# Kernel optimization log

Hardware: AMD Instinct MI355X
Metric: run time of the kernel (lower is better)

The kernel has to match this reference:

```python
import jax, jax.numpy as jnp
import numpy as np

B, S_CTX, S_Q, D_CTX, D_Q = 16, 2048, 2048, 1024, 1024
MASK_P = 0.1  # fraction of masked context positions


def setup_inputs() -> dict:
    key = jax.random.key(0)
    k1, k2, k3, k4 = jax.random.split(key, 4)
    context = jax.random.normal(k1, (B, S_CTX, D_CTX), dtype=jnp.float32)
    query = jax.random.normal(k2, (S_Q, B, D_Q), dtype=jnp.float32)  # [q_steps, batch, query_size]
    W = jax.random.normal(k3, (D_CTX, D_Q), dtype=jnp.float32)       # learned bilinear weights
    context_mask = jax.random.uniform(k4, (B, S_CTX)) < MASK_P       # True = masked position
    return {"context": context, "query": query, "W": W, "context_mask": context_mask}


def reference(context, query, W, context_mask):
    # scores[b, q, s] = context[b, s, :] @ W @ query[q, b, :]   (temp = 1.0, so no scaling)
    cw = jnp.einsum('bsd,de->bse', context, W)            # [B, S_ctx, D_q]
    scores = jnp.einsum('bse,qbe->bqs', cw, query)        # [B, S_q, S_ctx]
    neg = jnp.asarray(-1e30, scores.dtype)                # finite stand-in for -inf (NaN-safe)
    scores = jnp.where(context_mask[:, None, :], neg, scores)
    attn = jax.nn.softmax(scores, axis=2)                 # [B, S_q, S_ctx]
    # rows where the whole context is masked get attention zeroed out
    all_masked = jnp.all(context_mask, axis=1)[:, None, None]
    attn = jnp.where(all_masked, jnp.asarray(0.0, attn.dtype), attn)
    composition = jnp.einsum('bqs,bsd->qbd', attn, context)  # [S_q, B, D_ctx]
    attn_out = attn.transpose(1, 0, 2)                       # [S_q, B, S_ctx]
    return attn_out, composition
```

## Files before the change

kernel.cpp:

```cpp
#include <hip/hip_runtime.h>
#include <cmath>

#define B_  16
#define SEQ 2048
#define DIM 1024
#define LDST 40

typedef short  short8 __attribute__((ext_vector_type(8)));
typedef float  f32x4  __attribute__((ext_vector_type(4)));

__device__ __forceinline__ unsigned short f2bf(float x) {
  unsigned u = __builtin_bit_cast(unsigned, x);
  return (unsigned short)((u + 0x7fffu + ((u >> 16) & 1u)) >> 16);
}
__device__ __forceinline__ float bf2f(unsigned short h) {
  unsigned u = ((unsigned)h) << 16;
  return __builtin_bit_cast(float, u);
}

__device__ __forceinline__ void gl16(const void* g, void* l) {
  __builtin_amdgcn_global_load_lds(
      (const __attribute__((address_space(1))) void*)g,
      (__attribute__((address_space(3))) void*)l, 16, 0, 0);
}

__global__ __launch_bounds__(256) void cvt_ctx(const float* __restrict__ X,
                                               unsigned short* __restrict__ hi,
                                               unsigned short* __restrict__ lo) {
  const size_t N8 = (size_t)B_ * SEQ * DIM / 8;
  for (size_t i = (size_t)blockIdx.x * 256 + threadIdx.x; i < N8;
       i += (size_t)gridDim.x * 256) {
    const size_t base = i * 8;
    float4 a = *(const float4*)&X[base];
    float4 c = *(const float4*)&X[base + 4];
    const float xs[8] = {a.x, a.y, a.z, a.w, c.x, c.y, c.z, c.w};
    short8 h, l;
#pragma unroll
    for (int j = 0; j < 8; ++j) {
      unsigned short hh = f2bf(xs[j]);
      h[j] = (short)hh;
      l[j] = (short)f2bf(xs[j] - bf2f(hh));
    }
    *(short8*)&hi[base] = h;
    *(short8*)&lo[base] = l;
  }
}

__global__ __launch_bounds__(256) void g1_z(const float* __restrict__ Q,
                                            const float* __restrict__ W,
                                            unsigned short* __restrict__ zhi,
                                            unsigned short* __restrict__ zlo) {
  __shared__ unsigned short Ah[128 * LDST], Al[128 * LDST];
  __shared__ unsigned short Bh[128 * LDST], Bl[128 * LDST];
  const int tid = threadIdx.x;
  const int m0 = blockIdx.y * 128, n0 = blockIdx.x * 128;
  const int wave = tid >> 6, lane = tid & 63;
  const int wm = (wave >> 1) * 64, wn = (wave & 1) * 64;
  const int rl = tid & 127;

  const float* srow = (tid < 128) ? Q + (size_t)(m0 + rl) * DIM
                                  : W + (size_t)(n0 + rl) * DIM;
  unsigned short* th = (tid < 128) ? Ah : Bh;
  unsigned short* tl = (tid < 128) ? Al : Bl;

  f32x4 acc[4][4];
#pragma unroll
  for (int i = 0; i < 4; ++i)
#pragma unroll
    for (int j = 0; j < 4; ++j) acc[i][j] = (f32x4){0.f, 0.f, 0.f, 0.f};

  for (int kc = 0; kc < DIM; kc += 32) {
    float4 fv[8];
#pragma unroll
    for (int j = 0; j < 8; ++j) fv[j] = *(const float4*)&srow[kc + j * 4];
    __syncthreads();
    short8 hv[4], lv[4];
#pragma unroll
    for (int j = 0; j < 8; ++j) {
      const float x[4] = {fv[j].x, fv[j].y, fv[j].z, fv[j].w};
#pragma unroll
      for (int c = 0; c < 4; ++c) {
        unsigned short h = f2bf(x[c]);
        unsigned short l = f2bf(x[c] - bf2f(h));
        hv[j >> 1][(j & 1) * 4 + c] = (short)h;
        lv[j >> 1][(j & 1) * 4 + c] = (short)l;
      }
    }
#pragma unroll
    for (int j = 0; j < 4; ++j) {
      *(short8*)&th[rl * LDST + j * 8] = hv[j];
      *(short8*)&tl[rl * LDST + j * 8] = lv[j];
    }
    __syncthreads();

    short8 ah[4], al[4], bh[4], bl[4];
#pragma unroll
    for (int f = 0; f < 4; ++f) {
      const int ao = (wm + f * 16 + (lane & 15)) * LDST + (lane >> 4) * 8;
      const int bo = (wn + f * 16 + (lane & 15)) * LDST + (lane >> 4) * 8;
      ah[f] = *(const short8*)&Ah[ao];  al[f] = *(const short8*)&Al[ao];
      bh[f] = *(const short8*)&Bh[bo];  bl[f] = *(const short8*)&Bl[bo];
    }
#pragma unroll
    for (int i = 0; i < 4; ++i)
#pragma unroll
      for (int j = 0; j < 4; ++j) {
        acc[i][j] = __builtin_amdgcn_mfma_f32_16x16x32_bf16(ah[i], bh[j], acc[i][j], 0, 0, 0);
        acc[i][j] = __builtin_amdgcn_mfma_f32_16x16x32_bf16(al[i], bh[j], acc[i][j], 0, 0, 0);
        acc[i][j] = __builtin_amdgcn_mfma_f32_16x16x32_bf16(ah[i], bl[j], acc[i][j], 0, 0, 0);
      }
  }
#pragma unroll
  for (int i = 0; i < 4; ++i)
#pragma unroll
    for (int j = 0; j < 4; ++j)
#pragma unroll
      for (int r = 0; r < 4; ++r) {
        const int row = m0 + wm + i * 16 + (lane >> 4) * 4 + r;
        const int col = n0 + wn + j * 16 + (lane & 15);
        const float v = acc[i][j][r];
        const unsigned short h = f2bf(v);
        zhi[(size_t)row * DIM + col] = h;
        zlo[(size_t)row * DIM + col] = f2bf(v - bf2f(h));
      }
}

#define G2GRID (16 * 16 * B_)
__global__ __launch_bounds__(256) void g2_scores(const unsigned short* __restrict__ zhi,
                                                 const unsigned short* __restrict__ zlo,
                                                 const unsigned short* __restrict__ chi,
                                                 const unsigned short* __restrict__ clo,
                                                 float* __restrict__ Sc) {
  __shared__ unsigned short Sh[128 * 32], Sl[128 * 32];
  __shared__ unsigned short Qh[128 * 32], Ql[128 * 32];
  const int tid = threadIdx.x, lane = tid & 63, wave = tid >> 6;

  const int lin = blockIdx.x;
  const int swz = (lin & 7) * (G2GRID / 8) + (lin >> 3);
  const int s0 = (swz & 15) * 128;
  const int q0 = ((swz >> 4) & 15) * 128;
  const int b  = swz >> 8;

  const int wm = (wave >> 1) * 64;
  const int wn = (wave & 1) * 64;

  const int r_sub = lane >> 2;
  const int c_sub = (lane & 3) * 8;

  f32x4 acc[4][4];
#pragma unroll
  for (int i = 0; i < 4; ++i)
#pragma unroll
    for (int j = 0; j < 4; ++j) acc[i][j] = (f32x4){0.f, 0.f, 0.f, 0.f};

  for (int kc = 0; kc < DIM; kc += 32) {
    if (wave == 0) {
#pragma unroll
      for (int it = 0; it < 8; ++it)
        gl16(&chi[((size_t)b * SEQ + s0 + it * 16 + r_sub) * DIM + kc + c_sub], &Sh[it * 512]);
    } else if (wave == 1) {
#pragma unroll
      for (int it = 0; it < 8; ++it)
        gl16(&clo[((size_t)b * SEQ + s0 + it * 16 + r_sub) * DIM + kc + c_sub], &Sl[it * 512]);
    } else if (wave == 2) {
#pragma unroll
      for (int it = 0; it < 8; ++it)
        gl16(&zhi[((size_t)(q0 + it * 16 + r_sub) * B_ + b) * DIM + kc + c_sub], &Qh[it * 512]);
    } else {
#pragma unroll
      for (int it = 0; it < 8; ++it)
        gl16(&zlo[((size_t)(q0 + it * 16 + r_sub) * B_ + b) * DIM + kc + c_sub], &Ql[it * 512]);
    }
    __syncthreads();

    const int fo = lane & 15, fk = (lane >> 4) * 8;
    short8 sh_[4], sl_[4], qh_[4], ql_[4];
#pragma unroll
    for (int f = 0; f < 4; ++f) {
      const int so = (wm + f * 16 + fo) * 32 + fk;
      const int qo = (wn + f * 16 + fo) * 32 + fk;
      sh_[f] = *(const short8*)&Sh[so];  sl_[f] = *(const short8*)&Sl[so];
      qh_[f] = *(const short8*)&Qh[qo];  ql_[f] = *(const short8*)&Ql[qo];
    }
#pragma unroll
    for (int i = 0; i < 4; ++i)
#pragma unroll
      for (int j = 0; j < 4; ++j) {
        acc[i][j] = __builtin_amdgcn_mfma_f32_16x16x32_bf16(sh_[i], qh_[j], acc[i][j], 0, 0, 0);
        acc[i][j] = __builtin_amdgcn_mfma_f32_16x16x32_bf16(sl_[i], qh_[j], acc[i][j], 0, 0, 0);
        acc[i][j] = __builtin_amdgcn_mfma_f32_16x16x32_bf16(sh_[i], ql_[j], acc[i][j], 0, 0, 0);
      }
    __syncthreads();
  }

#pragma unroll
  for (int i = 0; i < 4; ++i)
#pragma unroll
    for (int j = 0; j < 4; ++j) {
      const int s = s0 + wm + i * 16 + (lane >> 4) * 4;
      const int q = q0 + wn + j * 16 + (lane & 15);
      f32x4 v = {acc[i][j][0], acc[i][j][1], acc[i][j][2], acc[i][j][3]};
      __builtin_nontemporal_store(v, (f32x4*)&Sc[((size_t)q * B_ + b) * SEQ + s]);
    }
}

__global__ __launch_bounds__(256) void kernel_softmax(float* __restrict__ attn,
                                                      const int* __restrict__ mask,
                                                      unsigned short* __restrict__ attnb) {
  const int row = blockIdx.x;
  const int b = row & (B_ - 1);
  const int q = row >> 4;
  float* p = attn + (size_t)row * SEQ;
  const int* m = mask + (size_t)b * SEQ;
  unsigned short* pb = attnb + ((size_t)b * SEQ + q) * SEQ;
  const int t = threadIdx.x;

  float v[8];
  float mx = -INFINITY;
#pragma unroll
  for (int i = 0; i < 8; ++i) {
    const int s = t + i * 256;
    float x = p[s];
    x = m[s] ? -1e30f : x;
    v[i] = x;
    mx = fmaxf(mx, x);
  }
#pragma unroll
  for (int off = 32; off > 0; off >>= 1) mx = fmaxf(mx, __shfl_xor(mx, off));
  __shared__ float redmax[4];
  __shared__ float redsum[4];
  if ((t & 63) == 0) redmax[t >> 6] = mx;
  __syncthreads();
  mx = fmaxf(fmaxf(redmax[0], redmax[1]), fmaxf(redmax[2], redmax[3]));

  float sum = 0.f;
#pragma unroll
  for (int i = 0; i < 8; ++i) {
    v[i] = __expf(v[i] - mx);
    sum += v[i];
  }
#pragma unroll
  for (int off = 32; off > 0; off >>= 1) sum += __shfl_xor(sum, off);
  if ((t & 63) == 0) redsum[t >> 6] = sum;
  __syncthreads();
  sum = (redsum[0] + redsum[1]) + (redsum[2] + redsum[3]);

  const bool allmasked = (mx < -1e29f);
  const float inv = allmasked ? 0.f : 1.f / sum;
#pragma unroll
  for (int i = 0; i < 8; ++i) {
    const float a = v[i] * inv;
    p[t + i * 256] = a;
    pb[t + i * 256] = f2bf(a);
  }
}

__global__ __launch_bounds__(256) void g3_comp(const unsigned short* __restrict__ attnb,
                                               const float* __restrict__ Ctx,
                                               float* __restrict__ Out) {
  __shared__ unsigned short As[128 * LDST], Bs[128 * LDST];
  const int b = blockIdx.z;
  const int tid = threadIdx.x;
  const int q0 = blockIdx.y * 128, d0 = blockIdx.x * 128;
  const int wave = tid >> 6, lane = tid & 63;
  const int wm = (wave >> 1) * 64, wn = (wave & 1) * 64;

  const int arow = tid >> 1, ak = (tid & 1) * 16;
  const int dl = tid & 127, sh = tid >> 7;

  const unsigned short* asrc = attnb + ((size_t)b * SEQ + (q0 + arow)) * SEQ + ak;
  const float* bsrc = Ctx + (size_t)b * SEQ * DIM + d0 + dl;

  f32x4 acc[4][4];
#pragma unroll
  for (int i = 0; i < 4; ++i)
#pragma unroll
    for (int j = 0; j < 4; ++j) acc[i][j] = (f32x4){0.f, 0.f, 0.f, 0.f};

  for (int kc = 0; kc < SEQ; kc += 32) {
    int4 a0 = *(const int4*)&asrc[kc];
    int4 a1 = *(const int4*)&asrc[kc + 8];
    float bf[16];
#pragma unroll
    for (int i = 0; i < 16; ++i)
      bf[i] = bsrc[(size_t)(kc + sh * 16 + i) * DIM];
    __syncthreads();
    *(int4*)&As[arow * LDST + ak]     = a0;
    *(int4*)&As[arow * LDST + ak + 8] = a1;
    short8 bv[2];
#pragma unroll
    for (int i = 0; i < 16; ++i) bv[i >> 3][i & 7] = (short)f2bf(bf[i]);
    *(short8*)&Bs[dl * LDST + sh * 16]     = bv[0];
    *(short8*)&Bs[dl * LDST + sh * 16 + 8] = bv[1];
    __syncthreads();

    short8 af[4], bfr[4];
#pragma unroll
    for (int f = 0; f < 4; ++f) {
      af[f]  = *(const short8*)&As[(wm + f * 16 + (lane & 15)) * LDST + (lane >> 4) * 8];
      bfr[f] = *(const short8*)&Bs[(wn + f * 16 + (lane & 15)) * LDST + (lane >> 4) * 8];
    }
#pragma unroll
    for (int i = 0; i < 4; ++i)
#pragma unroll
      for (int j = 0; j < 4; ++j)
        acc[i][j] = __builtin_amdgcn_mfma_f32_16x16x32_bf16(af[i], bfr[j], acc[i][j], 0, 0, 0);
  }
#pragma unroll
  for (int i = 0; i < 4; ++i)
#pragma unroll
    for (int j = 0; j < 4; ++j)
#pragma unroll
      for (int r = 0; r < 4; ++r) {
        const int q = q0 + wm + i * 16 + (lane >> 4) * 4 + r;
        const int d = d0 + wn + j * 16 + (lane & 15);
        Out[((size_t)q * B_ + b) * DIM + d] = acc[i][j][r];
      }
}

extern "C" void kernel_launch(void* const* d_in, const int* in_sizes, int n_in,
                              void* d_out, int out_size, void* d_ws, size_t ws_size,
                              hipStream_t stream) {
  const float* context = (const float*)d_in[0];
  const float* query   = (const float*)d_in[1];
  const float* W       = (const float*)d_in[2];
  const int*   mask    = (const int*)d_in[3];

  float* attn = (float*)d_out;
  float* comp = attn + (size_t)SEQ * B_ * SEQ;

  unsigned short* chi = (unsigned short*)comp;
  unsigned short* clo = chi + (size_t)B_ * SEQ * DIM;

  unsigned short* zhi   = (unsigned short*)d_ws;
  unsigned short* zlo   = zhi + (size_t)SEQ * B_ * DIM;
  unsigned short* attnb = (unsigned short*)d_ws;

  cvt_ctx<<<dim3(4096), 256, 0, stream>>>(context, chi, clo);
  g1_z<<<dim3(DIM / 128, (SEQ * B_) / 128), 256, 0, stream>>>(query, W, zhi, zlo);
  g2_scores<<<dim3(G2GRID), 256, 0, stream>>>(zhi, zlo, chi, clo, attn);
  kernel_softmax<<<dim3(SEQ * B_), 256, 0, stream>>>(attn, mask, attnb);
  g3_comp<<<dim3(DIM / 128, SEQ / 128, B_), 256, 0, stream>>>(attnb, context, comp);
}
```

Measured before the change: 1.197 ms.

## Transpose context to bf16 and read fp32 attention directly in composition GEMM

A new kernel pre-transposes the context into a bf16 [B, D, S] buffer. The composition GEMM then loads it into LDS with async global-to-LDS copies and converts fp32 attention rows to bf16 in-kernel, instead of softmax writing a separate bf16 attention copy. XOR swizzling of LDS columns is added to both the scores and composition GEMMs to reduce bank conflicts, and the composition output is written with vectorized nontemporal stores. This trades the bf16 attention write for an extra transpose pass over the context and a re-read of fp32 attention.

```diff
diff --git a/kernel.cpp b/kernel.cpp
--- a/kernel.cpp
+++ b/kernel.cpp
@@ -7,6 +7,7 @@
 #define LDST 40
 
 typedef short  short8 __attribute__((ext_vector_type(8)));
+typedef short  sh4    __attribute__((ext_vector_type(4)));
 typedef float  f32x4  __attribute__((ext_vector_type(4)));
 
 __device__ __forceinline__ unsigned short f2bf(float x) {
@@ -46,6 +47,28 @@
   }
 }
 
+__global__ __launch_bounds__(256) void t_ctx(const float* __restrict__ X,
+                                             unsigned short* __restrict__ T) {
+  __shared__ unsigned short L[64 * 72];
+  const int t = threadIdx.x;
+  const int d0 = blockIdx.x * 64, s0 = blockIdx.y * 64, b = blockIdx.z;
+#pragma unroll
+  for (int p = 0; p < 4; ++p) {
+    const int sl = (t >> 4) + p * 16, d4 = (t & 15) * 4;
+    float4 v = *(const float4*)&X[((size_t)b * SEQ + s0 + sl) * DIM + d0 + d4];
+    sh4 o = {(short)f2bf(v.x), (short)f2bf(v.y), (short)f2bf(v.z), (short)f2bf(v.w)};
+    *(sh4*)&L[sl * 72 + d4] = o;
+  }
+  __syncthreads();
+#pragma unroll
+  for (int p = 0; p < 4; ++p) {
+    const int dl = (t >> 4) + p * 16, s4 = (t & 15) * 4;
+    sh4 o = {(short)L[(s4 + 0) * 72 + dl], (short)L[(s4 + 1) * 72 + dl],
+             (short)L[(s4 + 2) * 72 + dl], (short)L[(s4 + 3) * 72 + dl]};
+    *(sh4*)&T[((size_t)b * DIM + d0 + dl) * SEQ + s0 + s4] = o;
+  }
+}
+
 __global__ __launch_bounds__(256) void g1_z(const float* __restrict__ Q,
                                             const float* __restrict__ W,
                                             unsigned short* __restrict__ zhi,
@@ -145,7 +168,7 @@
   const int wn = (wave & 1) * 64;
 
   const int r_sub = lane >> 2;
-  const int c_sub = (lane & 3) * 8;
+  const int c_sub = (((lane & 3) ^ ((lane >> 3) & 3))) * 8;
 
   f32x4 acc[4][4];
 #pragma unroll
@@ -173,12 +196,13 @@
     }
     __syncthreads();
 
-    const int fo = lane & 15, fk = (lane >> 4) * 8;
     short8 sh_[4], sl_[4], qh_[4], ql_[4];
 #pragma unroll
     for (int f = 0; f < 4; ++f) {
-      const int so = (wm + f * 16 + fo) * 32 + fk;
-      const int qo = (wn + f * 16 + fo) * 32 + fk;
+      const int ra = wm + f * 16 + (lane & 15);
+      const int rb = wn + f * 16 + (lane & 15);
+      const int so = ra * 32 + (((lane >> 4) ^ ((ra >> 1) & 3))) * 8;
+      const int qo = rb * 32 + (((lane >> 4) ^ ((rb >> 1) & 3))) * 8;
       sh_[f] = *(const short8*)&Sh[so];  sl_[f] = *(const short8*)&Sl[so];
       qh_[f] = *(const short8*)&Qh[qo];  ql_[f] = *(const short8*)&Ql[qo];
     }
@@ -205,14 +229,11 @@
 }
 
 __global__ __launch_bounds__(256) void kernel_softmax(float* __restrict__ attn,
-                                                      const int* __restrict__ mask,
-                                                      unsigned short* __restrict__ attnb) {
+                                                      const int* __restrict__ mask) {
   const int row = blockIdx.x;
   const int b = row & (B_ - 1);
-  const int q = row >> 4;
   float* p = attn + (size_t)row * SEQ;
   const int* m = mask + (size_t)b * SEQ;
-  unsigned short* pb = attnb + ((size_t)b * SEQ + q) * SEQ;
   const int t = threadIdx.x;
 
   float v[8];
@@ -248,28 +269,29 @@
   const bool allmasked = (mx < -1e29f);
   const float inv = allmasked ? 0.f : 1.f / sum;
 #pragma unroll
-  for (int i = 0; i < 8; ++i) {
-    const float a = v[i] * inv;
-    p[t + i * 256] = a;
-    pb[t + i * 256] = f2bf(a);
-  }
-}
-
-__global__ __launch_bounds__(256) void g3_comp(const unsigned short* __restrict__ attnb,
-                                               const float* __restrict__ Ctx,
+  for (int i = 0; i < 8; ++i) p[t + i * 256] = v[i] * inv;
+}
+
+__global__ __launch_bounds__(256) void g3_comp(const float* __restrict__ attn,
+                                               const unsigned short* __restrict__ ctxT,
                                                float* __restrict__ Out) {
-  __shared__ unsigned short As[128 * LDST], Bs[128 * LDST];
+  __shared__ unsigned short Ad[128 * 32];
+  __shared__ unsigned short Bq[128 * 32];
+  const int tid = threadIdx.x, lane = tid & 63, wave = tid >> 6;
   const int b = blockIdx.z;
-  const int tid = threadIdx.x;
-  const int q0 = blockIdx.y * 128, d0 = blockIdx.x * 128;
-  const int wave = tid >> 6, lane = tid & 63;
-  const int wm = (wave >> 1) * 64, wn = (wave & 1) * 64;
-
-  const int arow = tid >> 1, ak = (tid & 1) * 16;
-  const int dl = tid & 127, sh = tid >> 7;
-
-  const unsigned short* asrc = attnb + ((size_t)b * SEQ + (q0 + arow)) * SEQ + ak;
-  const float* bsrc = Ctx + (size_t)b * SEQ * DIM + d0 + dl;
+  const int d0 = blockIdx.x * 128, q0 = blockIdx.y * 128;
+  const int wm = (wave >> 1) * 64;
+  const int wn = (wave & 1) * 64;
+
+  const int r_sub = lane >> 2;
+  const int c_sub = (((lane & 3) ^ ((lane >> 3) & 3))) * 8;
+
+  const int qrow = tid >> 1, shalf = (tid & 1) * 16;
+  const float* arow = attn + ((size_t)(q0 + qrow) * B_ + b) * SEQ;
+  const int qsw = (qrow >> 1) & 3;
+  const int blk_base = (tid & 1) * 2;
+  unsigned short* bdst0 = &Bq[qrow * 32 + ((blk_base + 0) ^ qsw) * 8];
+  unsigned short* bdst1 = &Bq[qrow * 32 + ((blk_base + 1) ^ qsw) * 8];
 
   f32x4 acc[4][4];
 #pragma unroll
@@ -278,44 +300,54 @@
     for (int j = 0; j < 4; ++j) acc[i][j] = (f32x4){0.f, 0.f, 0.f, 0.f};
 
   for (int kc = 0; kc < SEQ; kc += 32) {
-    int4 a0 = *(const int4*)&asrc[kc];
-    int4 a1 = *(const int4*)&asrc[kc + 8];
-    float bf[16];
-#pragma unroll
-    for (int i = 0; i < 16; ++i)
-      bf[i] = bsrc[(size_t)(kc + sh * 16 + i) * DIM];
-    __syncthreads();
-    *(int4*)&As[arow * LDST + ak]     = a0;
-    *(int4*)&As[arow * LDST + ak + 8] = a1;
-    short8 bv[2];
-#pragma unroll
-    for (int i = 0; i < 16; ++i) bv[i >> 3][i & 7] = (short)f2bf(bf[i]);
-    *(short8*)&Bs[dl * LDST + sh * 16]     = bv[0];
-    *(short8*)&Bs[dl * LDST + sh * 16 + 8] = bv[1];
-    __syncthreads();
-
-    short8 af[4], bfr[4];
+    float4 fv[4];
+#pragma unroll
+    for (int j = 0; j < 4; ++j) fv[j] = *(const float4*)&arow[kc + shalf + j * 4];
+#pragma unroll
+    for (int i = 0; i < 2; ++i) {
+      const int rb = wave * 32 + i * 16;
+      gl16(&ctxT[((size_t)b * DIM + d0 + rb + r_sub) * SEQ + kc + c_sub], &Ad[rb * 32]);
+    }
+    short8 bv0, bv1;
+#pragma unroll
+    for (int j = 0; j < 4; ++j) {
+      const float x[4] = {fv[j].x, fv[j].y, fv[j].z, fv[j].w};
+#pragma unroll
+      for (int c = 0; c < 4; ++c) {
+        const int e = j * 4 + c;
+        if (e < 8) bv0[e] = (short)f2bf(x[c]);
+        else       bv1[e - 8] = (short)f2bf(x[c]);
+      }
+    }
+    *(short8*)bdst0 = bv0;
+    *(short8*)bdst1 = bv1;
+    __syncthreads();
+
+    short8 af[4], bf_[4];
 #pragma unroll
     for (int f = 0; f < 4; ++f) {
-      af[f]  = *(const short8*)&As[(wm + f * 16 + (lane & 15)) * LDST + (lane >> 4) * 8];
-      bfr[f] = *(const short8*)&Bs[(wn + f * 16 + (lane & 15)) * LDST + (lane >> 4) * 8];
+      const int ra = wm + f * 16 + (lane & 15);
+      const int rb = wn + f * 16 + (lane & 15);
+      af[f]  = *(const short8*)&Ad[ra * 32 + (((lane >> 4) ^ ((ra >> 1) & 3))) * 8];
+      bf_[f] = *(const short8*)&Bq[rb * 32 + (((lane >> 4) ^ ((rb >> 1) & 3))) * 8];
     }
 #pragma unroll
     for (int i = 0; i < 4; ++i)
 #pragma unroll
       for (int j = 0; j < 4; ++j)
-        acc[i][j] = __builtin_amdgcn_mfma_f32_16x16x32_bf16(af[i], bfr[j], acc[i][j], 0, 0, 0);
-  }
-#pragma unroll
-  for (int i = 0; i < 4; ++i)
-#pragma unroll
-    for (int j = 0; j < 4; ++j)
-#pragma unroll
-      for (int r = 0; r < 4; ++r) {
-        const int q = q0 + wm + i * 16 + (lane >> 4) * 4 + r;
-        const int d = d0 + wn + j * 16 + (lane & 15);
-        Out[((size_t)q * B_ + b) * DIM + d] = acc[i][j][r];
-      }
+        acc[i][j] = __builtin_amdgcn_mfma_f32_16x16x32_bf16(af[i], bf_[j], acc[i][j], 0, 0, 0);
+    __syncthreads();
+  }
+
+#pragma unroll
+  for (int i = 0; i < 4; ++i)
+#pragma unroll
+    for (int j = 0; j < 4; ++j) {
+      const int d = d0 + wm + i * 16 + (lane >> 4) * 4;
+      const int q = q0 + wn + j * 16 + (lane & 15);
+      f32x4 v = {acc[i][j][0], acc[i][j][1], acc[i][j][2], acc[i][j][3]};
+      __builtin_nontemporal_store(v, (f32x4*)&Out[((size_t)q * B_ + b) * DIM + d]);
+    }
 }
 
 extern "C" void kernel_launch(void* const* d_in, const int* in_sizes, int n_in,
@@ -332,13 +364,14 @@
   unsigned short* chi = (unsigned short*)comp;
   unsigned short* clo = chi + (size_t)B_ * SEQ * DIM;
 
-  unsigned short* zhi   = (unsigned short*)d_ws;
-  unsigned short* zlo   = zhi + (size_t)SEQ * B_ * DIM;
-  unsigned short* attnb = (unsigned short*)d_ws;
+  unsigned short* zhi  = (unsigned short*)d_ws;
+  unsigned short* zlo  = zhi + (size_t)SEQ * B_ * DIM;
+  unsigned short* ctxT = (unsigned short*)d_ws;
 
   cvt_ctx<<<dim3(4096), 256, 0, stream>>>(context, chi, clo);
   g1_z<<<dim3(DIM / 128, (SEQ * B_) / 128), 256, 0, stream>>>(query, W, zhi, zlo);
   g2_scores<<<dim3(G2GRID), 256, 0, stream>>>(zhi, zlo, chi, clo, attn);
-  kernel_softmax<<<dim3(SEQ * B_), 256, 0, stream>>>(attn, mask, attnb);
-  g3_comp<<<dim3(DIM / 128, SEQ / 128, B_), 256, 0, stream>>>(attnb, context, comp);
-}
+  t_ctx<<<dim3(DIM / 64, SEQ / 64, B_), 256, 0, stream>>>(context, ctxT);
+  kernel_softmax<<<dim3(SEQ * B_), 256, 0, stream>>>(attn, mask);
+  g3_comp<<<dim3(DIM / 128, SEQ / 128, B_), 256, 0, stream>>>(attn, ctxT, comp);
+}
```

Result: slower. 1.258 ms (+5.1%).
